# Optimization experiments

Measured on AMD Instinct MI355X. Metric: run time of the kernel, lower is better.

## Reference

```python
import jax, jax.numpy as jnp
import numpy as np

HIDDEN = 128
NUM_RADIAL = 16
NUM_DENSE = 3
OUT_DIM = 1
N_NODES = 50000
N_EDGES = 600000


def setup_inputs() -> dict:
    key = jax.random.key(0)
    ks = jax.random.split(key, 16)
    h = jax.random.normal(ks[0], (N_NODES, HIDDEN), dtype=jnp.float32)
    radial_basis = jax.random.normal(ks[1], (N_EDGES, NUM_RADIAL), dtype=jnp.float32)
    edge_index = jax.random.randint(ks[2], (2, N_EDGES), 0, N_NODES, dtype=jnp.int32)

    def lin(k, fan_in, fan_out):
        bound = 1.0 / np.sqrt(fan_in)
        kw, kb = jax.random.split(k)
        W = jax.random.uniform(kw, (fan_in, fan_out), minval=-bound, maxval=bound, dtype=jnp.float32)
        b = jax.random.uniform(kb, (fan_out,), minval=-bound, maxval=bound, dtype=jnp.float32)
        return W, b

    rW1, rb1 = lin(ks[3], NUM_RADIAL, HIDDEN)
    rW2, rb2 = lin(ks[4], HIDDEN, HIDDEN)
    dW, db = [], []
    for i in range(NUM_DENSE):
        W, b = lin(ks[5 + i], HIDDEN, HIDDEN)
        dW.append(W); db.append(b)
    oW, ob = lin(ks[10], HIDDEN, OUT_DIM)
    return {
        "h": h, "radial_basis": radial_basis, "edge_index": edge_index,
        "rW1": rW1, "rb1": rb1, "rW2": rW2, "rb2": rb2,
        "dW0": dW[0], "db0": db[0], "dW1": dW[1], "db1": db[1], "dW2": dW[2], "db2": db[2],
        "oW": oW, "ob": ob,
    }


def reference(h, radial_basis, edge_index, rW1, rb1, rW2, rb2,
              dW0, db0, dW1, db1, dW2, db2, oW, ob):
    src, dst = edge_index[0], edge_index[1]
    # radial_net: Linear -> SiLU -> Linear, output [n_edges, hidden]
    W = jax.nn.silu(radial_basis @ rW1 + rb1) @ rW2 + rb2
    # gather -> multiply -> scatter-add (message passing)
    h_edge = h[src] * W                      # [n_edges, hidden]
    x = jax.ops.segment_sum(h_edge, dst, num_segments=h.shape[0])  # [n_atoms, hidden]
    # dense layers
    for dw, dbias in ((dW0, db0), (dW1, db1), (dW2, db2)):
        x = jax.nn.silu(x @ dw + dbias)
    return x @ oW + ob                        # [n_atoms, output_dim]
```

## Files before the change

### kernel.cpp

```cpp
#include <hip/hip_runtime.h>

typedef short bf16x8 __attribute__((ext_vector_type(8)));
typedef float f32x4 __attribute__((ext_vector_type(4)));
typedef float f32x2 __attribute__((ext_vector_type(2)));
typedef unsigned int u32x4 __attribute__((ext_vector_type(4)));

__device__ __forceinline__ unsigned short f2bf(float f) {
  unsigned int u = __float_as_uint(f);
  u = (u + 0x7FFFu + ((u >> 16) & 1u)) >> 16;
  return (unsigned short)u;
}
__device__ __forceinline__ float bf2f(unsigned short u) {
  return __uint_as_float(((unsigned int)u) << 16);
}
__device__ __forceinline__ float silu_f(float v) {
  return v * (1.0f / (1.0f + __expf(-v)));
}
__device__ __forceinline__ unsigned int pkbf(float a, float b) {
  unsigned int r;
  asm("v_cvt_pk_bf16_f32 %0, %1, %2" : "=v"(r) : "v"(a), "v"(b));
  return r;
}
__device__ __forceinline__ void st2bf(char* base, int byA, int byB, float a, float b) {
  unsigned int p = pkbf(a, b);
  *(unsigned short*)(base + byA) = (unsigned short)p;
  *(unsigned short*)(base + byB) = (unsigned short)(p >> 16);
}

__global__ void k_prep(const float* __restrict__ rW1, const float* __restrict__ rb1,
                       const float* __restrict__ rW2, const float* __restrict__ dW0,
                       const float* __restrict__ dW1, const float* __restrict__ dW2,
                       unsigned short* __restrict__ wb, int* __restrict__ hist,
                       int nzero) {
  int i = blockIdx.x * blockDim.x + threadIdx.x;
  if (i < 4096) {
    int j = i & 7, lane = (i >> 3) & 63, nt = i >> 9;
    int k = (lane >> 4) * 8 + j, n = nt * 16 + (lane & 15);
    float v = (k < 16) ? rW1[k * 128 + n] : (k == 16 ? rb1[n] : 0.0f);
    wb[i] = f2bf(v);
  } else if (i < 4096 + 4 * 16384) {
    int i2 = i - 4096, buf = i2 >> 14, r = i2 & 16383;
    int j = r & 7, lane = (r >> 3) & 63, g = r >> 9, kc = g & 3, nt = g >> 2;
    int k = kc * 32 + (lane >> 4) * 8 + j, n = nt * 16 + (lane & 15);
    const float* W = (buf == 0) ? rW2 : (buf == 1) ? dW0 : (buf == 2) ? dW1 : dW2;
    wb[4096 + buf * 16384 + r] = f2bf(W[k * 128 + n]);
  } else if (i - 69632 < nzero) {
    hist[i - 69632] = 0;
  }
}

__global__ void k_hist(const int* __restrict__ ei, int* __restrict__ hist, int E) {
  int e = blockIdx.x * blockDim.x + threadIdx.x;
  if (e < E) atomicAdd(&hist[ei[E + e]], 1);
}

__global__ __launch_bounds__(1024) void k_scanA(const int* __restrict__ hist,
                                                int* __restrict__ part, int N) {
  __shared__ int red[1024];
  const int t = threadIdx.x;
  const int i = blockIdx.x * 1024 + t;
  red[t] = (i < N) ? hist[i] : 0;
  __syncthreads();
  for (int o = 512; o; o >>= 1) {
    if (t < o) red[t] += red[t + o];
    __syncthreads();
  }
  if (t == 0) part[blockIdx.x] = red[0];
}

__global__ __launch_bounds__(1024) void k_scanC(
    const int* __restrict__ hist, const int* __restrict__ part,
    int* __restrict__ row_start, int* __restrict__ bump, int N, int nb) {
  __shared__ int sh[1024];
  __shared__ int s_off;
  const int t = threadIdx.x;
  const int b = blockIdx.x;
  if (t < 64) {
    int p = (t < nb) ? part[t] : 0;
#pragma unroll
    for (int o = 1; o < 64; o <<= 1) {
      int u = __shfl_up(p, o);
      if (t >= o) p += u;
    }
    if (b == 0) {
      if (t == 0) s_off = 0;
    } else if (t == b - 1) {
      s_off = p;
    }
  }
  __syncthreads();
  const int i = b * 1024 + t;
  const int v = (i < N) ? hist[i] : 0;
  sh[t] = v;
  __syncthreads();
  for (int o = 1; o < 1024; o <<= 1) {
    int u = (t >= o) ? sh[t - o] : 0;
    __syncthreads();
    sh[t] += u;
    __syncthreads();
  }
  const int excl = s_off + sh[t] - v;
  if (i < N) {
    row_start[i] = excl;
    bump[i] = excl;
  } else if (i == N) {
    row_start[N] = excl;
  }
}

__global__ void k_pos(const int* __restrict__ ei, int* __restrict__ bump,
                      int* __restrict__ pos, int E) {
  int e = blockIdx.x * blockDim.x + threadIdx.x;
  if (e < E) pos[e] = atomicAdd(&bump[ei[E + e]], 1);
}

__global__ __launch_bounds__(256, 2) void k_edge2(
    const float* __restrict__ rb, const int* __restrict__ ei,
    const float* __restrict__ h, const unsigned short* __restrict__ B1,
    const unsigned short* __restrict__ B2, const float* __restrict__ rb2,
    const int* __restrict__ pos, unsigned short* __restrict__ Mbuf,
    int E, int ntiles) {
  const int lane = threadIdx.x & 63;
  const int wid = threadIdx.x >> 6;
  const int kg = lane >> 4;
  const int c15 = lane & 15;
  __shared__ __align__(16) unsigned short hid[64 * 128];

  bf16x8 b2f[8][4];
#pragma unroll
  for (int nt = 0; nt < 8; ++nt)
#pragma unroll
    for (int kc = 0; kc < 4; ++kc)
      b2f[nt][kc] = *(const bf16x8*)(B2 + (((nt * 4 + kc) * 64 + lane) << 3));

  float rb2r[8];
#pragma unroll
  for (int nt = 0; nt < 8; ++nt) rb2r[nt] = rb2[nt * 16 + c15];

  for (int t = blockIdx.x; t < ntiles; t += gridDim.x) {
    const int ebase = t * 64 + wid * 16;

    bf16x8 a1 = {};
    if (kg < 2) {
      const int e = ebase + c15;
      if (e < E) {
        const f32x4 v0 = __builtin_nontemporal_load((const f32x4*)(rb + (size_t)e * 16 + kg * 8));
        const f32x4 v1 = __builtin_nontemporal_load((const f32x4*)(rb + (size_t)e * 16 + kg * 8 + 4));
        unsigned int p0 = pkbf(v0[0], v0[1]), p1 = pkbf(v0[2], v0[3]);
        unsigned int p2 = pkbf(v1[0], v1[1]), p3 = pkbf(v1[2], v1[3]);
        a1[0] = (short)(p0 & 0xffff); a1[1] = (short)(p0 >> 16);
        a1[2] = (short)(p1 & 0xffff); a1[3] = (short)(p1 >> 16);
        a1[4] = (short)(p2 & 0xffff); a1[5] = (short)(p2 >> 16);
        a1[6] = (short)(p3 & 0xffff); a1[7] = (short)(p3 >> 16);
      }
    } else if (kg == 2) {
      a1[0] = (short)0x3F80;
    }

#pragma unroll
    for (int nt = 0; nt < 8; ++nt) {
      bf16x8 b1 = *(const bf16x8*)(B1 + ((nt * 64 + lane) << 3));
      f32x4 d1 = {};
      d1 = __builtin_amdgcn_mfma_f32_16x16x32_bf16(a1, b1, d1, 0, 0, 0);
#pragma unroll
      for (int r = 0; r < 4; r += 2) {
        const int row0 = wid * 16 + kg * 4 + r;
        const int row1 = row0 + 1;
        const int col2 = (nt * 16 + c15) * 2;
        st2bf((char*)hid,
              (row0 * 256 + col2) ^ ((row0 & 7) << 4),
              (row1 * 256 + col2) ^ ((row1 & 7) << 4),
              silu_f(d1[r]), silu_f(d1[r + 1]));
      }
    }

    const int arow = wid * 16 + c15;
    f32x4 acc[8] = {};
#pragma unroll
    for (int kc = 0; kc < 4; ++kc) {
      int byt = arow * 256 + (kc * 32 + kg * 8) * 2;
      byt ^= (arow & 7) << 4;
      const bf16x8 a2 = *(const bf16x8*)((const char*)hid + byt);
#pragma unroll
      for (int nt = 0; nt < 8; ++nt)
        acc[nt] = __builtin_amdgcn_mfma_f32_16x16x32_bf16(a2, b2f[nt][kc], acc[nt], 0, 0, 0);
    }

#pragma unroll
    for (int nt = 0; nt < 8; ++nt)
#pragma unroll
      for (int r = 0; r < 4; r += 2) {
        const int row0 = wid * 16 + kg * 4 + r;
        const int row1 = row0 + 1;
        const int col2 = (nt * 16 + c15) * 2;
        st2bf((char*)hid,
              (row0 * 256 + col2) ^ ((row0 & 7) << 4),
              (row1 * 256 + col2) ^ ((row1 & 7) << 4),
              acc[nt][r] + rb2r[nt], acc[nt][r + 1] + rb2r[nt]);
      }

#pragma unroll
    for (int pass = 0; pass < 2; ++pass) {
      const int ro = wid * 16 + pass * 8 + (lane >> 3);
      const int e = t * 64 + ro;
      if (e < E) {
        const int p = pos[e];
        const int s = ei[e];
        const int cg = (lane & 7) * 16;
        const int swz = (ro & 7) << 4;
        const int bas = ro * 256 + cg * 2;
        const bf16x8 w0 = *(const bf16x8*)((const char*)hid + (bas ^ swz));
        const bf16x8 w1 = *(const bf16x8*)((const char*)hid + ((bas + 16) ^ swz));
        const f32x4* hp = (const f32x4*)(h + (size_t)s * 128 + cg);
        const f32x4 h0 = hp[0], h1 = hp[1], h2 = hp[2], h3 = hp[3];
        u32x4 m0, m1;
        m0[0] = pkbf(bf2f((unsigned short)w0[0]) * h0[0], bf2f((unsigned short)w0[1]) * h0[1]);
        m0[1] = pkbf(bf2f((unsigned short)w0[2]) * h0[2], bf2f((unsigned short)w0[3]) * h0[3]);
        m0[2] = pkbf(bf2f((unsigned short)w0[4]) * h1[0], bf2f((unsigned short)w0[5]) * h1[1]);
        m0[3] = pkbf(bf2f((unsigned short)w0[6]) * h1[2], bf2f((unsigned short)w0[7]) * h1[3]);
        m1[0] = pkbf(bf2f((unsigned short)w1[0]) * h2[0], bf2f((unsigned short)w1[1]) * h2[1]);
        m1[1] = pkbf(bf2f((unsigned short)w1[2]) * h2[2], bf2f((unsigned short)w1[3]) * h2[3]);
        m1[2] = pkbf(bf2f((unsigned short)w1[4]) * h3[0], bf2f((unsigned short)w1[5]) * h3[1]);
        m1[3] = pkbf(bf2f((unsigned short)w1[6]) * h3[2], bf2f((unsigned short)w1[7]) * h3[3]);
        *(u32x4*)(Mbuf + (size_t)p * 128 + cg) = m0;
        *(u32x4*)(Mbuf + (size_t)p * 128 + cg + 8) = m1;
      }
    }
  }
}

__device__ __forceinline__ void dense_silu_layer(
    unsigned short* xt, const unsigned short* __restrict__ W,
    const float* __restrict__ bias, int wid, int kg, int c15, int lane) {
  const int arow = wid * 16 + c15;
  f32x4 acc[8] = {};
#pragma unroll
  for (int kc = 0; kc < 4; ++kc) {
    int byt = arow * 256 + (kc * 32 + kg * 8) * 2;
    byt ^= (arow & 7) << 4;
    const bf16x8 a2 = *(const bf16x8*)((const char*)xt + byt);
#pragma unroll
    for (int nt = 0; nt < 8; ++nt) {
      const bf16x8 bf = *(const bf16x8*)(W + (((nt * 4 + kc) * 64 + lane) << 3));
      acc[nt] = __builtin_amdgcn_mfma_f32_16x16x32_bf16(a2, bf, acc[nt], 0, 0, 0);
    }
  }
#pragma unroll
  for (int nt = 0; nt < 8; ++nt) {
    const float b = bias[nt * 16 + c15];
#pragma unroll
    for (int r = 0; r < 4; r += 2) {
      const int row0 = wid * 16 + kg * 4 + r;
      const int row1 = row0 + 1;
      const int col2 = (nt * 16 + c15) * 2;
      st2bf((char*)xt,
            (row0 * 256 + col2) ^ ((row0 & 7) << 4),
            (row1 * 256 + col2) ^ ((row1 & 7) << 4),
            silu_f(acc[nt][r] + b), silu_f(acc[nt][r + 1] + b));
    }
  }
}

__global__ __launch_bounds__(512) void k_gtile(
    const unsigned short* __restrict__ Mbuf, const int* __restrict__ row_start,
    const unsigned short* __restrict__ Dw, const float* __restrict__ db0,
    const float* __restrict__ db1, const float* __restrict__ db2,
    const float* __restrict__ oW, const float* __restrict__ ob,
    float* __restrict__ out, int NN, int tiles) {
  const int tid = threadIdx.x;
  const int lane = tid & 63;
  const int wid = tid >> 6;
  const int kg = lane >> 4;
  const int c15 = lane & 15;
  __shared__ __align__(16) unsigned short xt[128 * 128];

  for (int t = blockIdx.x; t < tiles; t += gridDim.x) {
    if (t != (int)blockIdx.x) __syncthreads();
    const int rbase = wid * 16;
    const int nbase = t * 128 + rbase;

    for (int i = 0; i < 16; i += 2) {
      const int nA = nbase + i, nB = nbase + i + 1;
      int a0 = 0, a1 = 0, b0 = 0, b1 = 0;
      if (nA < NN) { a0 = row_start[nA]; a1 = row_start[nA + 1]; }
      if (nB < NN) { b0 = row_start[nB]; b1 = row_start[nB + 1]; }
      const int lenA = a1 - a0, lenB = b1 - b0;
      const int maxlen = lenA > lenB ? lenA : lenB;
      float sa[8] = {}, sb[8] = {};
      for (int off = kg; off < maxlen; off += 4) {
        if (off < lenA) {
          const bf16x8 v = *(const bf16x8*)(Mbuf + (size_t)(a0 + off) * 128 + c15 * 8);
#pragma unroll
          for (int k = 0; k < 8; ++k) sa[k] += bf2f((unsigned short)v[k]);
        }
        if (off < lenB) {
          const bf16x8 v = *(const bf16x8*)(Mbuf + (size_t)(b0 + off) * 128 + c15 * 8);
#pragma unroll
          for (int k = 0; k < 8; ++k) sb[k] += bf2f((unsigned short)v[k]);
        }
      }
#pragma unroll
      for (int k = 0; k < 8; ++k) {
        float s = sa[k];
        s += __shfl_xor(s, 16);
        s += __shfl_xor(s, 32);
        sa[k] = s;
        float q = sb[k];
        q += __shfl_xor(q, 16);
        q += __shfl_xor(q, 32);
        sb[k] = q;
      }
      if (kg == 0) {
        if (nA < NN) {
          const int row = rbase + i;
          u32x4 w;
          w[0] = pkbf(sa[0], sa[1]); w[1] = pkbf(sa[2], sa[3]);
          w[2] = pkbf(sa[4], sa[5]); w[3] = pkbf(sa[6], sa[7]);
          const int byt = (row * 256 + c15 * 16) ^ ((row & 7) << 4);
          *(u32x4*)((char*)xt + byt) = w;
        }
      } else if (kg == 1) {
        if (nB < NN) {
          const int row = rbase + i + 1;
          u32x4 w;
          w[0] = pkbf(sb[0], sb[1]); w[1] = pkbf(sb[2], sb[3]);
          w[2] = pkbf(sb[4], sb[5]); w[3] = pkbf(sb[6], sb[7]);
          const int byt = (row * 256 + c15 * 16) ^ ((row & 7) << 4);
          *(u32x4*)((char*)xt + byt) = w;
        }
      }
    }

    __syncthreads();

    dense_silu_layer(xt, Dw, db0, wid, kg, c15, lane);
    dense_silu_layer(xt, Dw + 16384, db1, wid, kg, c15, lane);

    {
      const int arow = wid * 16 + c15;
      const unsigned short* W = Dw + 32768;
      f32x4 acc[8] = {};
#pragma unroll
      for (int kc = 0; kc < 4; ++kc) {
        int byt = arow * 256 + (kc * 32 + kg * 8) * 2;
        byt ^= (arow & 7) << 4;
        const bf16x8 a2 = *(const bf16x8*)((const char*)xt + byt);
#pragma unroll
        for (int nt = 0; nt < 8; ++nt) {
          const bf16x8 bf = *(const bf16x8*)(W + (((nt * 4 + kc) * 64 + lane) << 3));
          acc[nt] = __builtin_amdgcn_mfma_f32_16x16x32_bf16(a2, bf, acc[nt], 0, 0, 0);
        }
      }
      const float obv = ob[0];
#pragma unroll
      for (int r = 0; r < 4; ++r) {
        float p = 0.f;
#pragma unroll
        for (int nt = 0; nt < 8; ++nt) {
          const float b = db2[nt * 16 + c15];
          p += silu_f(acc[nt][r] + b) * oW[nt * 16 + c15];
        }
        p += __shfl_xor(p, 1);
        p += __shfl_xor(p, 2);
        p += __shfl_xor(p, 4);
        p += __shfl_xor(p, 8);
        const int n = nbase + kg * 4 + r;
        if (c15 == 0 && n < NN) out[n] = p + obv;
      }
    }
  }
}

__global__ __launch_bounds__(256, 2) void k_edge(
    const float* __restrict__ rb, const int* __restrict__ ei,
    const float* __restrict__ h, const unsigned short* __restrict__ B1,
    const unsigned short* __restrict__ B2, const float* __restrict__ rb2,
    float* __restrict__ x, int E, int ntiles) {
  const int lane = threadIdx.x & 63;
  const int wid = threadIdx.x >> 6;
  const int kg = lane >> 4;
  const int c15 = lane & 15;
  __shared__ __align__(16) unsigned short hid[64 * 128];

  bf16x8 b2f[8][4];
#pragma unroll
  for (int nt = 0; nt < 8; ++nt)
#pragma unroll
    for (int kc = 0; kc < 4; ++kc)
      b2f[nt][kc] = *(const bf16x8*)(B2 + (((nt * 4 + kc) * 64 + lane) << 3));

  float rb2r[8];
#pragma unroll
  for (int nt = 0; nt < 8; ++nt) rb2r[nt] = rb2[nt * 16 + c15];

  for (int t = blockIdx.x; t < ntiles; t += gridDim.x) {
    const int ebase = t * 64 + wid * 16;
    bf16x8 a1 = {};
    if (kg < 2) {
      const int e = ebase + c15;
      if (e < E) {
        const f32x4 v0 = *(const f32x4*)(rb + (size_t)e * 16 + kg * 8);
        const f32x4 v1 = *(const f32x4*)(rb + (size_t)e * 16 + kg * 8 + 4);
        a1[0] = (short)f2bf(v0[0]); a1[1] = (short)f2bf(v0[1]);
        a1[2] = (short)f2bf(v0[2]); a1[3] = (short)f2bf(v0[3]);
        a1[4] = (short)f2bf(v1[0]); a1[5] = (short)f2bf(v1[1]);
        a1[6] = (short)f2bf(v1[2]); a1[7] = (short)f2bf(v1[3]);
      }
    } else if (kg == 2) {
      a1[0] = (short)0x3F80;
    }
#pragma unroll
    for (int nt = 0; nt < 8; ++nt) {
      bf16x8 b1 = *(const bf16x8*)(B1 + ((nt * 64 + lane) << 3));
      f32x4 d1 = {};
      d1 = __builtin_amdgcn_mfma_f32_16x16x32_bf16(a1, b1, d1, 0, 0, 0);
#pragma unroll
      for (int r = 0; r < 4; ++r) {
        const int row = wid * 16 + kg * 4 + r;
        int byt = row * 256 + (nt * 16 + c15) * 2;
        byt ^= (row & 7) << 4;
        *(unsigned short*)((char*)hid + byt) = f2bf(silu_f(d1[r]));
      }
    }
    const int arow = wid * 16 + c15;
    f32x4 acc[8] = {};
#pragma unroll
    for (int kc = 0; kc < 4; ++kc) {
      int byt = arow * 256 + (kc * 32 + kg * 8) * 2;
      byt ^= (arow & 7) << 4;
      const bf16x8 a2 = *(const bf16x8*)((const char*)hid + byt);
#pragma unroll
      for (int nt = 0; nt < 8; ++nt)
        acc[nt] = __builtin_amdgcn_mfma_f32_16x16x32_bf16(a2, b2f[nt][kc], acc[nt], 0, 0, 0);
    }
#pragma unroll
    for (int r = 0; r < 4; ++r) {
      const int e = ebase + kg * 4 + r;
      if (e < E) {
        const int s = ei[e];
        const int d = ei[E + e];
#pragma unroll
        for (int nt = 0; nt < 8; ++nt) {
          const int col = nt * 16 + c15;
          const float w = acc[nt][r] + rb2r[nt];
          const float hv = h[(size_t)s * 128 + col];
          atomicAdd(x + (size_t)d * 128 + col, w * hv);
        }
      }
    }
  }
}

__global__ __launch_bounds__(256, 2) void k_dense(
    float* __restrict__ x, const unsigned short* __restrict__ Bw,
    const float* __restrict__ bias, int M) {
  const int lane = threadIdx.x & 63;
  const int wid = threadIdx.x >> 6;
  const int kg = lane >> 4;
  const int c15 = lane & 15;

  bf16x8 bf[8][4];
#pragma unroll
  for (int nt = 0; nt < 8; ++nt)
#pragma unroll
    for (int kc = 0; kc < 4; ++kc)
      bf[nt][kc] = *(const bf16x8*)(Bw + (((nt * 4 + kc) * 64 + lane) << 3));

  float br[8];
#pragma unroll
  for (int nt = 0; nt < 8; ++nt) br[nt] = bias[nt * 16 + c15];

  const int tiles = (M + 63) >> 6;
  for (int t = blockIdx.x; t < tiles; t += gridDim.x) {
    const int rbase = t * 64 + wid * 16;
    const int row = rbase + c15;
    bf16x8 a[4];
#pragma unroll
    for (int kc = 0; kc < 4; ++kc) {
      bf16x8 az = {};
      if (row < M) {
        const f32x4 v0 = *(const f32x4*)(x + (size_t)row * 128 + kc * 32 + kg * 8);
        const f32x4 v1 = *(const f32x4*)(x + (size_t)row * 128 + kc * 32 + kg * 8 + 4);
        az[0] = (short)f2bf(v0[0]); az[1] = (short)f2bf(v0[1]);
        az[2] = (short)f2bf(v0[2]); az[3] = (short)f2bf(v0[3]);
        az[4] = (short)f2bf(v1[0]); az[5] = (short)f2bf(v1[1]);
        az[6] = (short)f2bf(v1[2]); az[7] = (short)f2bf(v1[3]);
      }
      a[kc] = az;
    }
    f32x4 acc[8] = {};
#pragma unroll
    for (int kc = 0; kc < 4; ++kc)
#pragma unroll
      for (int nt = 0; nt < 8; ++nt)
        acc[nt] = __builtin_amdgcn_mfma_f32_16x16x32_bf16(a[kc], bf[nt][kc], acc[nt], 0, 0, 0);
#pragma unroll
    for (int r = 0; r < 4; ++r) {
      const int orow = rbase + kg * 4 + r;
      if (orow < M) {
#pragma unroll
        for (int nt = 0; nt < 8; ++nt)
          x[(size_t)orow * 128 + nt * 16 + c15] = silu_f(acc[nt][r] + br[nt]);
      }
    }
  }
}

__global__ void k_out(const float* __restrict__ x, const float* __restrict__ oW,
                      const float* __restrict__ ob, float* __restrict__ out, int M) {
  const int lane = threadIdx.x & 63;
  const int w = (int)((blockIdx.x * blockDim.x + threadIdx.x) >> 6);
  const int nw = (int)((gridDim.x * blockDim.x) >> 6);
  const float w0 = oW[lane], w1 = oW[64 + lane];
  const float obv = ob[0];
  for (int row = w; row < M; row += nw) {
    float a = x[(size_t)row * 128 + lane] * w0 + x[(size_t)row * 128 + 64 + lane] * w1;
#pragma unroll
    for (int m = 32; m; m >>= 1) a += __shfl_xor(a, m);
    if (lane == 0) out[row] = a + obv;
  }
}

extern "C" void kernel_launch(void* const* d_in, const int* in_sizes, int n_in,
                              void* d_out, int out_size, void* d_ws, size_t ws_size,
                              hipStream_t stream) {
  const float* h   = (const float*)d_in[0];
  const float* rb  = (const float*)d_in[1];
  const int*   ei  = (const int*)d_in[2];
  const float* rW1 = (const float*)d_in[3];
  const float* rb1 = (const float*)d_in[4];
  const float* rW2 = (const float*)d_in[5];
  const float* rb2 = (const float*)d_in[6];
  const float* dW0 = (const float*)d_in[7];
  const float* db0 = (const float*)d_in[8];
  const float* dW1 = (const float*)d_in[9];
  const float* db1 = (const float*)d_in[10];
  const float* dW2 = (const float*)d_in[11];
  const float* db2 = (const float*)d_in[12];
  const float* oW  = (const float*)d_in[13];
  const float* ob  = (const float*)d_in[14];

  const int NN = in_sizes[0] / 128;
  const int E  = in_sizes[1] / 16;

  char* base = (char*)d_ws;
  size_t off = 0;
  auto alloc = [&](size_t bytes) {
    char* p = base + off;
    off += (bytes + 255) & ~(size_t)255;
    return p;
  };
  float* x            = (float*)alloc((size_t)NN * 128 * 4);
  unsigned short* wb  = (unsigned short*)alloc((size_t)69632 * 2);
  int* row_start      = (int*)alloc((size_t)(NN + 1) * 4);
  int* hist           = (int*)alloc((size_t)NN * 4);
  int* bump           = (int*)alloc((size_t)NN * 4);
  int* part           = (int*)alloc((size_t)64 * 4);
  int* pos            = (int*)alloc((size_t)E * 4);
  unsigned short* Mb  = (unsigned short*)alloc((size_t)E * 256);
  const bool fits = off <= ws_size && NN <= 65535;

  const int ntiles = (E + 63) / 64;
  const int gE = (E + 255) / 256;
  const int nb = (NN + 1023) / 1024;

  if (fits) {
    k_prep<<<(69632 + NN + 255) / 256, 256, 0, stream>>>(rW1, rb1, rW2, dW0, dW1,
                                                         dW2, wb, hist, NN);
    k_hist<<<gE, 256, 0, stream>>>(ei, hist, E);
    k_scanA<<<nb, 1024, 0, stream>>>(hist, part, NN);
    k_scanC<<<nb, 1024, 0, stream>>>(hist, part, row_start, bump, NN, nb);
    k_pos<<<gE, 256, 0, stream>>>(ei, bump, pos, E);
    const int eg = ntiles < 2048 ? ntiles : 2048;
    k_edge2<<<eg, 256, 0, stream>>>(rb, ei, h, wb, wb + 4096, rb2, pos, Mb, E, ntiles);
    const int gt = (NN + 127) / 128;
    k_gtile<<<gt, 512, 0, stream>>>(Mb, row_start, wb + 20480, db0, db1, db2,
                                    oW, ob, (float*)d_out, NN, gt);
  } else {
    k_prep<<<(69632 + 255) / 256, 256, 0, stream>>>(rW1, rb1, rW2, dW0, dW1,
                                                    dW2, wb, hist, 0);
    hipMemsetAsync(x, 0, (size_t)NN * 512, stream);
    const int eg = ntiles < 1024 ? ntiles : 1024;
    k_edge<<<eg, 256, 0, stream>>>(rb, ei, h, wb, wb + 4096, rb2, x, E, ntiles);
    k_dense<<<512, 256, 0, stream>>>(x, wb + 20480, db0, NN);
    k_dense<<<512, 256, 0, stream>>>(x, wb + 36864, db1, NN);
    k_dense<<<512, 256, 0, stream>>>(x, wb + 53248, db2, NN);
    k_out<<<512, 256, 0, stream>>>(x, oW, ob, (float*)d_out, NN);
  }
}
```

Before: 306.2 us.

## Fuse slot assignment into edge kernel and gather four nodes per iteration

Removes the separate k_pos kernel and the pos array. Each edge row now takes its CSR slot with an atomicAdd on bump inside k_edge2, made by one lane of each group of eight and broadcast with a shuffle. This saves a launch and a full pass over edges. The gather loop in k_gtile now handles four nodes per iteration, one per kg lane group, so more loads are in flight and no lane group sits idle. The cost is more atomics inside the edge kernel and more registers held in the gather loop.

```diff
diff --git a/kernel.cpp b/kernel.cpp
--- a/kernel.cpp
+++ b/kernel.cpp
@@ -108,17 +108,11 @@
   }
 }
 
-__global__ void k_pos(const int* __restrict__ ei, int* __restrict__ bump,
-                      int* __restrict__ pos, int E) {
-  int e = blockIdx.x * blockDim.x + threadIdx.x;
-  if (e < E) pos[e] = atomicAdd(&bump[ei[E + e]], 1);
-}
-
 __global__ __launch_bounds__(256, 2) void k_edge2(
     const float* __restrict__ rb, const int* __restrict__ ei,
     const float* __restrict__ h, const unsigned short* __restrict__ B1,
     const unsigned short* __restrict__ B2, const float* __restrict__ rb2,
-    const int* __restrict__ pos, unsigned short* __restrict__ Mbuf,
+    int* __restrict__ bump, unsigned short* __restrict__ Mbuf,
     int E, int ntiles) {
   const int lane = threadIdx.x & 63;
   const int wid = threadIdx.x >> 6;
@@ -204,7 +198,10 @@
       const int ro = wid * 16 + pass * 8 + (lane >> 3);
       const int e = t * 64 + ro;
       if (e < E) {
-        const int p = pos[e];
+        const int d = ei[E + e];
+        int pc = 0;
+        if ((lane & 7) == 0) pc = atomicAdd(&bump[d], 1);
+        const int p = __shfl(pc, lane & 56);
         const int s = ei[e];
         const int cg = (lane & 7) * 16;
         const int swz = (ro & 7) << 4;
@@ -279,54 +276,57 @@
     const int rbase = wid * 16;
     const int nbase = t * 128 + rbase;
 
-    for (int i = 0; i < 16; i += 2) {
-      const int nA = nbase + i, nB = nbase + i + 1;
-      int a0 = 0, a1 = 0, b0 = 0, b1 = 0;
-      if (nA < NN) { a0 = row_start[nA]; a1 = row_start[nA + 1]; }
-      if (nB < NN) { b0 = row_start[nB]; b1 = row_start[nB + 1]; }
-      const int lenA = a1 - a0, lenB = b1 - b0;
-      const int maxlen = lenA > lenB ? lenA : lenB;
-      float sa[8] = {}, sb[8] = {};
+    for (int i = 0; i < 16; i += 4) {
+      int base[4], len[4];
+#pragma unroll
+      for (int j = 0; j < 4; ++j) {
+        const int n = nbase + i + j;
+        if (n < NN) {
+          const int b0 = row_start[n];
+          base[j] = b0;
+          len[j] = row_start[n + 1] - b0;
+        } else {
+          base[j] = 0;
+          len[j] = 0;
+        }
+      }
+      int maxlen = len[0] > len[1] ? len[0] : len[1];
+      maxlen = maxlen > len[2] ? maxlen : len[2];
+      maxlen = maxlen > len[3] ? maxlen : len[3];
+      float s[4][8] = {};
       for (int off = kg; off < maxlen; off += 4) {
-        if (off < lenA) {
-          const bf16x8 v = *(const bf16x8*)(Mbuf + (size_t)(a0 + off) * 128 + c15 * 8);
-#pragma unroll
-          for (int k = 0; k < 8; ++k) sa[k] += bf2f((unsigned short)v[k]);
-        }
-        if (off < lenB) {
-          const bf16x8 v = *(const bf16x8*)(Mbuf + (size_t)(b0 + off) * 128 + c15 * 8);
-#pragma unroll
-          for (int k = 0; k < 8; ++k) sb[k] += bf2f((unsigned short)v[k]);
-        }
-      }
-#pragma unroll
-      for (int k = 0; k < 8; ++k) {
-        float s = sa[k];
-        s += __shfl_xor(s, 16);
-        s += __shfl_xor(s, 32);
-        sa[k] = s;
-        float q = sb[k];
-        q += __shfl_xor(q, 16);
-        q += __shfl_xor(q, 32);
-        sb[k] = q;
-      }
-      if (kg == 0) {
-        if (nA < NN) {
-          const int row = rbase + i;
-          u32x4 w;
-          w[0] = pkbf(sa[0], sa[1]); w[1] = pkbf(sa[2], sa[3]);
-          w[2] = pkbf(sa[4], sa[5]); w[3] = pkbf(sa[6], sa[7]);
-          const int byt = (row * 256 + c15 * 16) ^ ((row & 7) << 4);
-          *(u32x4*)((char*)xt + byt) = w;
-        }
-      } else if (kg == 1) {
-        if (nB < NN) {
-          const int row = rbase + i + 1;
-          u32x4 w;
-          w[0] = pkbf(sb[0], sb[1]); w[1] = pkbf(sb[2], sb[3]);
-          w[2] = pkbf(sb[4], sb[5]); w[3] = pkbf(sb[6], sb[7]);
-          const int byt = (row * 256 + c15 * 16) ^ ((row & 7) << 4);
-          *(u32x4*)((char*)xt + byt) = w;
+#pragma unroll
+        for (int j = 0; j < 4; ++j) {
+          if (off < len[j]) {
+            const bf16x8 v = *(const bf16x8*)(Mbuf + (size_t)(base[j] + off) * 128 + c15 * 8);
+#pragma unroll
+            for (int k = 0; k < 8; ++k) s[j][k] += bf2f((unsigned short)v[k]);
+          }
+        }
+      }
+#pragma unroll
+      for (int j = 0; j < 4; ++j)
+#pragma unroll
+        for (int k = 0; k < 8; ++k) {
+          float v = s[j][k];
+          v += __shfl_xor(v, 16);
+          v += __shfl_xor(v, 32);
+          s[j][k] = v;
+        }
+#pragma unroll
+      for (int j = 0; j < 4; ++j) {
+        if (kg == j) {
+          const int n = nbase + i + j;
+          if (n < NN) {
+            const int row = rbase + i + j;
+            u32x4 w;
+            w[0] = pkbf(s[j][0], s[j][1]);
+            w[1] = pkbf(s[j][2], s[j][3]);
+            w[2] = pkbf(s[j][4], s[j][5]);
+            w[3] = pkbf(s[j][6], s[j][7]);
+            const int byt = (row * 256 + c15 * 16) ^ ((row & 7) << 4);
+            *(u32x4*)((char*)xt + byt) = w;
+          }
         }
       }
     }
@@ -556,7 +556,6 @@
   int* hist           = (int*)alloc((size_t)NN * 4);
   int* bump           = (int*)alloc((size_t)NN * 4);
   int* part           = (int*)alloc((size_t)64 * 4);
-  int* pos            = (int*)alloc((size_t)E * 4);
   unsigned short* Mb  = (unsigned short*)alloc((size_t)E * 256);
   const bool fits = off <= ws_size && NN <= 65535;
 
@@ -570,9 +569,8 @@
     k_hist<<<gE, 256, 0, stream>>>(ei, hist, E);
     k_scanA<<<nb, 1024, 0, stream>>>(hist, part, NN);
     k_scanC<<<nb, 1024, 0, stream>>>(hist, part, row_start, bump, NN, nb);
-    k_pos<<<gE, 256, 0, stream>>>(ei, bump, pos, E);
     const int eg = ntiles < 2048 ? ntiles : 2048;
-    k_edge2<<<eg, 256, 0, stream>>>(rb, ei, h, wb, wb + 4096, rb2, pos, Mb, E, ntiles);
+    k_edge2<<<eg, 256, 0, stream>>>(rb, ei, h, wb, wb + 4096, rb2, bump, Mb, E, ntiles);
     const int gt = (NN + 127) / 128;
     k_gtile<<<gt, 512, 0, stream>>>(Mb, row_start, wb + 20480, db0, db1, db2,
                                     oW, ob, (float*)d_out, NN, gt);
```

Measured after the change: 299.4 us. 2.2% less time.
